# Kernel optimization log

Hardware: AMD Instinct MI355X
Metric: run time of the kernel (lower is better)

The kernel has to match this reference:

```python
import jax, jax.numpy as jnp
import numpy as np

NUM_QUBITS = 12
NUM_LAYERS = 4
N_CLASSES = 10
BATCH = 512
BN_EPS = 1e-5


def _apply_1q(state, U, wire):
    """Apply a 1-qubit gate U on `wire`. state: (B,)+(2,)*n; U: (2,2) or (B,2,2)."""
    state = jnp.moveaxis(state, wire + 1, -1)
    if U.ndim == 3:
        out = jnp.einsum('bij,b...j->b...i', U, state)
    else:
        out = jnp.einsum('ij,b...j->b...i', U, state)
    return jnp.moveaxis(out, -1, wire + 1)


def _apply_cnot(state, ctrl, tgt):
    s = jnp.moveaxis(state, (ctrl + 1, tgt + 1), (-2, -1))
    # where control bit == 1, flip the target axis
    s = jnp.concatenate([s[..., 0:1, :], s[..., 1:2, ::-1]], axis=-2)
    return jnp.moveaxis(s, (-2, -1), (ctrl + 1, tgt + 1))


def _rot(phi, theta, omega):
    """PennyLane Rot(phi, theta, omega) = RZ(omega) RY(theta) RZ(phi)."""
    c = jnp.cos(theta / 2)
    s = jnp.sin(theta / 2)
    row0 = jnp.stack([jnp.exp(-1j * (phi + omega) / 2) * c,
                      -jnp.exp(1j * (phi - omega) / 2) * s])
    row1 = jnp.stack([jnp.exp(-1j * (phi - omega) / 2) * s,
                      jnp.exp(1j * (phi + omega) / 2) * c])
    return jnp.stack([row0, row1]).astype(jnp.complex64)


def _circuit(x, weights):
    """Batched state-vector sim of the data-reuploading VQC.
    x: (B, n_qubits) angles; weights: (L, n_qubits, 3). Returns (B, N_CLASSES) <Z_i>."""
    B = x.shape[0]
    state = jnp.zeros((B,) + (2,) * NUM_QUBITS, jnp.complex64)
    state = state.at[(slice(None),) + (0,) * NUM_QUBITS].set(1.0)
    half = (x * 0.5).astype(jnp.float32)
    for l in range(NUM_LAYERS):
        w = weights[l]
        # angle embedding (RY(x_q) on each wire) -- batched gate, differs per sample
        for q in range(NUM_QUBITS):
            c = jnp.cos(half[:, q])
            s = jnp.sin(half[:, q])
            U = jnp.stack([jnp.stack([c, -s], -1),
                           jnp.stack([s, c], -1)], -2).astype(jnp.complex64)  # (B,2,2)
            state = _apply_1q(state, U, q)
        # one StronglyEntangling layer: Rot per wire (shared across batch)
        for q in range(NUM_QUBITS):
            state = _apply_1q(state, _rot(w[q, 0], w[q, 1], w[q, 2]), q)
        # ring of CNOTs (range 1)
        for q in range(NUM_QUBITS):
            state = _apply_cnot(state, q, (q + 1) % NUM_QUBITS)
    probs = jnp.abs(state) ** 2  # (B,)+(2,)*n, float32
    all_axes = tuple(range(1, NUM_QUBITS + 1))
    expz = []
    for i in range(N_CLASSES):
        axes = tuple(a for a in all_axes if a != i + 1)
        p = probs.sum(axis=axes)  # (B, 2) marginal of qubit i
        expz.append(p[:, 0] - p[:, 1])
    return jnp.stack(expz, axis=-1)  # (B, N_CLASSES)


def setup_inputs() -> dict:
    key = jax.random.key(0)
    k1, k2 = jax.random.split(key)
    x = jax.random.normal(k1, (BATCH, NUM_QUBITS), dtype=jnp.float32)
    weights = 0.01 * jax.random.uniform(k2, (NUM_LAYERS, NUM_QUBITS, 3), dtype=jnp.float32)
    bias = jnp.zeros((N_CLASSES,), jnp.float32)
    gamma = jnp.ones((N_CLASSES,), jnp.float32)
    beta = jnp.zeros((N_CLASSES,), jnp.float32)
    return {"x": x, "weights": weights, "bias": bias, "gamma": gamma, "beta": beta}


def reference(x, weights, bias, gamma, beta):
    expz = _circuit(x, weights)
    probs = jax.nn.softmax(expz + bias, axis=-1)
    # BatchNorm1d (training mode): biased batch statistics, affine
    mu = probs.mean(axis=0)
    var = probs.var(axis=0)
    return (probs - mu) / jnp.sqrt(var + BN_EPS) * gamma + beta
```

## Files before the change

kernel.cpp:

```cpp
#include <hip/hip_runtime.h>
#include <math.h>

#define NQ 12
#define NL 4
#define NC 10
#define NB 512
#define BN_EPS 1e-5f

typedef float v2f __attribute__((ext_vector_type(2)));

__device__ __forceinline__ void bfly(v2f& A, v2f& B,
    v2f c0, v2f c1, v2f c2, v2f c3, v2f c4, v2f c5, v2f c6, v2f c7)
{
    const v2f As = A.yx, Bs = B.yx;
    const v2f An = __builtin_elementwise_fma(c0, A,
                   __builtin_elementwise_fma(c1, As,
                   __builtin_elementwise_fma(c2, B, c3 * Bs)));
    const v2f Bn = __builtin_elementwise_fma(c4, A,
                   __builtin_elementwise_fma(c5, As,
                   __builtin_elementwise_fma(c6, B, c7 * Bs)));
    A = An; B = Bn;
}

__global__ __launch_bounds__(256) void vqc_kernel(
    const float* __restrict__ x, const float* __restrict__ w,
    const float* __restrict__ bias, float* __restrict__ probs)
{
    __shared__ v2f buf[2][4096];
    __shared__ __align__(16) float gm[48][16];
    __shared__ float red[4*NC];

    const int b = blockIdx.x;
    const int t = threadIdx.x;

    if (t < 48) {
        const int l = t / NQ, q = t % NQ;
        const float xq = 0.5f * x[b*NQ + q];
        const float cx = cosf(xq), sx = sinf(xq);
        const int wi = (l*NQ + q)*3;
        const float phi = w[wi], tht = w[wi+1], om = w[wi+2];
        const float ct = cosf(0.5f*tht), st = sinf(0.5f*tht);
        const float aa = 0.5f*(phi + om), dd = 0.5f*(phi - om);
        const float ca = cosf(aa), sa = sinf(aa);
        const float cd = cosf(dd), sd = sinf(dd);
        const float u00r =  ca*ct, u00i = -sa*ct;
        const float u01r = -cd*st, u01i = -sd*st;
        const float u10r =  cd*st, u10i = -sd*st;
        const float u11r =  ca*ct, u11i =  sa*ct;
        const float m00r = u00r*cx + u01r*sx, m00i = u00i*cx + u01i*sx;
        const float m01r = u01r*cx - u00r*sx, m01i = u01i*cx - u00i*sx;
        const float m10r = u10r*cx + u11r*sx, m10i = u10i*cx + u11i*sx;
        const float m11r = u11r*cx - u10r*sx, m11i = u11i*cx - u10i*sx;
        float* gp = gm[t];
        gp[0]  =  m00r; gp[1]  = m00r;
        gp[2]  = -m00i; gp[3]  = m00i;
        gp[4]  =  m01r; gp[5]  = m01r;
        gp[6]  = -m01i; gp[7]  = m01i;
        gp[8]  =  m10r; gp[9]  = m10r;
        gp[10] = -m10i; gp[11] = m10i;
        gp[12] =  m11r; gp[13] = m11r;
        gp[14] = -m11i; gp[15] = m11i;
    }
    __syncthreads();

    v2f a[16];
    #pragma unroll
    for (int r = 0; r < 16; ++r) a[r] = (v2f){0.f, 0.f};
    if (t == 0) a[0].x = 1.f;

    const int tl = t & 15, th4 = t >> 4;
    const int phit = t ^ th4;
    const int vAB = (th4 << 8) | (tl ^ (th4 * 17));
    const int wBC = (tl << 8) | ((th4 ^ tl) * 17);

    const unsigned b0_ = t & 1u, b1_ = (t>>1)&1u, b2_ = (t>>2)&1u, b3_ = (t>>3)&1u,
                   b4_ = (t>>4)&1u, b5_ = (t>>5)&1u, b6_ = (t>>6)&1u, b7_ = (t>>7)&1u;
    const unsigned P7 = b7_, P6 = P7^b6_, P5 = P6^b5_, P4 = P5^b4_,
                   P3 = P4^b3_, P2 = P3^b2_, P1 = P2^b1_, T = P1^b0_;
    const unsigned base_j = ((T ^ b7_) << 11) | (P6 << 10) | (P5 << 9) | (P4 << 8)
                          | (P3 << 7) | (P2 << 6) | (P1 << 5) | (T << 4)
                          | (T ? 0xFu : 0u);
    const unsigned rA = (base_j >> 8) & 15u;
    const unsigned tA = base_j & 255u;
    const unsigned baseCA = (rA << 8) | ((tA ^ (tA >> 4)) ^ (rA * 17u));

    #define STAGE(base) \
        _Pragma("unroll") \
        for (int g = 0; g < 4; ++g) { \
            const v2f* cp = (const v2f*)gm[(base) + 3 - g]; \
            const v2f c0=cp[0],c1=cp[1],c2=cp[2],c3=cp[3], \
                      c4=cp[4],c5=cp[5],c6=cp[6],c7=cp[7]; \
            const int bit = 1 << g; \
            _Pragma("unroll") \
            for (int r0 = 0; r0 < 16; ++r0) \
                if (!(r0 & bit)) bfly(a[r0], a[r0|bit], c0,c1,c2,c3,c4,c5,c6,c7); \
        }

    int pb = 0;
    #pragma unroll
    for (int l = 0; l < NL; ++l) {
        STAGE(l*12)
        {
            v2f* bp = buf[pb]; pb ^= 1;
            #pragma unroll
            for (int r = 0; r < 16; ++r) bp[vAB ^ (r*17)] = a[r];
            __syncthreads();
            #pragma unroll
            for (int r = 0; r < 16; ++r) a[r] = bp[(r<<8) | (phit ^ (r*17))];
        }

        STAGE(l*12 + 4)
        {
            v2f* bp = buf[pb]; pb ^= 1;
            #pragma unroll
            for (int r = 0; r < 16; ++r) bp[wBC ^ r] = a[r];
            __syncthreads();
            #pragma unroll
            for (int r = 0; r < 16; ++r) a[r] = bp[(r<<8) | (phit ^ (r*17))];
        }

        STAGE(l*12 + 8)
        if (l < NL-1) {
            v2f* bp = buf[pb]; pb ^= 1;
            #pragma unroll
            for (int r = 0; r < 16; ++r) {
                const unsigned k3 = (r>>3)&1u;
                const unsigned k2 = k3 ^ ((r>>2)&1u);
                const unsigned k1 = k2 ^ ((r>>1)&1u);
                const unsigned k0 = k1 ^ (r&1u);
                const unsigned K  = (k3<<3)|(k2<<2)|(k1<<1)|k0;
                const unsigned d  = K ^ (k0 * 0x888u);
                bp[baseCA ^ d] = a[r];
            }
            __syncthreads();
            #pragma unroll
            for (int r = 0; r < 16; ++r) a[r] = bp[(r<<8) | (phit ^ (r*17))];
        }
    }

    const float S0 = (T ^ b7_) ? -1.f : 1.f;
    const float S1 = P6 ? -1.f : 1.f;
    const float S2 = P5 ? -1.f : 1.f;
    const float S3 = P4 ? -1.f : 1.f;
    const float S4 = P3 ? -1.f : 1.f;
    const float S5 = P2 ? -1.f : 1.f;
    const float S6 = P1 ? -1.f : 1.f;
    const float S7 = T  ? -1.f : 1.f;
    const float S8 = T  ? -1.f : 1.f;
    const float S9 = T  ? -1.f : 1.f;

    float acc[NC];
    #pragma unroll
    for (int c = 0; c < NC; ++c) acc[c] = 0.f;
    #pragma unroll
    for (int r = 0; r < 16; ++r) {
        const float p = a[r].x*a[r].x + a[r].y*a[r].y;
        const int r3 = (r>>3)&1, r2 = (r>>2)&1, r1 = (r>>1)&1, r0b = r&1;
        const int par = r3 ^ r2 ^ r1 ^ r0b;
        acc[0] += (par        ? -S0 : S0) * p;
        acc[1] += S1 * p;
        acc[2] += S2 * p;
        acc[3] += S3 * p;
        acc[4] += S4 * p;
        acc[5] += S5 * p;
        acc[6] += S6 * p;
        acc[7] += S7 * p;
        acc[8] += (r3         ? -S8 : S8) * p;
        acc[9] += ((r3 ^ r2)  ? -S9 : S9) * p;
    }
    #pragma unroll
    for (int off = 32; off >= 1; off >>= 1) {
        #pragma unroll
        for (int c = 0; c < NC; ++c)
            acc[c] += __shfl_down(acc[c], off, 64);
    }
    const int wave = t >> 6, lane = t & 63;
    if (lane == 0) {
        #pragma unroll
        for (int c = 0; c < NC; ++c) red[wave*NC + c] = acc[c];
    }
    __syncthreads();
    if (t == 0) {
        float ez[NC];
        float mx = -1e30f;
        #pragma unroll
        for (int c = 0; c < NC; ++c) {
            ez[c] = red[c] + red[NC + c] + red[2*NC + c] + red[3*NC + c] + bias[c];
            mx = fmaxf(mx, ez[c]);
        }
        float sum = 0.f;
        #pragma unroll
        for (int c = 0; c < NC; ++c) { ez[c] = expf(ez[c] - mx); sum += ez[c]; }
        const float inv = 1.f / sum;
        #pragma unroll
        for (int c = 0; c < NC; ++c) probs[b*NC + c] = ez[c] * inv;
    }
}

__global__ __launch_bounds__(256) void bn_kernel(
    float* __restrict__ probs, const float* __restrict__ gamma,
    const float* __restrict__ beta)
{
    const int c = blockIdx.x;
    const int t = threadIdx.x;
    const float v0 = probs[t*NC + c];
    const float v1 = probs[(t + 256)*NC + c];
    float s  = v0 + v1;
    float ss = v0*v0 + v1*v1;
    #pragma unroll
    for (int off = 32; off >= 1; off >>= 1) {
        s  += __shfl_down(s,  off, 64);
        ss += __shfl_down(ss, off, 64);
    }
    __shared__ float sm[8];
    __shared__ float stat[2];
    const int wave = t >> 6, lane = t & 63;
    if (lane == 0) { sm[wave] = s; sm[4 + wave] = ss; }
    __syncthreads();
    if (t == 0) {
        const float S  = sm[0] + sm[1] + sm[2] + sm[3];
        const float SS = sm[4] + sm[5] + sm[6] + sm[7];
        const float mu  = S * (1.f/512.f);
        const float var = SS * (1.f/512.f) - mu*mu;
        stat[0] = mu;
        stat[1] = 1.f / sqrtf(var + BN_EPS);
    }
    __syncthreads();
    const float mu = stat[0], inv = stat[1];
    const float g = gamma[c], bt = beta[c];
    probs[t*NC + c]         = (v0 - mu) * inv * g + bt;
    probs[(t + 256)*NC + c] = (v1 - mu) * inv * g + bt;
}

extern "C" void kernel_launch(void* const* d_in, const int* in_sizes, int n_in,
                              void* d_out, int out_size, void* d_ws, size_t ws_size,
                              hipStream_t stream) {
    const float* x     = (const float*)d_in[0];
    const float* w     = (const float*)d_in[1];
    const float* bias  = (const float*)d_in[2];
    const float* gamma = (const float*)d_in[3];
    const float* beta  = (const float*)d_in[4];
    float* out = (float*)d_out;

    vqc_kernel<<<NB, 256, 0, stream>>>(x, w, bias, out);
    bn_kernel<<<NC, 256, 0, stream>>>(out, gamma, beta);
}
```

Baseline: 85.75 us.

## Use 512 threads per sample and precompute fused gates in a separate kernel

The state-vector simulation now runs with 512 threads per block, each holding 8 amplitudes instead of 16, so qubits are processed in groups of three with four LDS transposes per layer and new swizzle patterns. The per-sample fused gate matrices are computed by a new gates_kernel into workspace and read from global memory, rather than computed by 48 threads while the rest of the block waits. This aims to cut register pressure, raise occupancy and remove the serial gate-setup phase. In exchange it adds a kernel launch, a global round trip for gate coefficients and one more barrier-separated shuffle per layer.

```diff
diff --git a/kernel.cpp b/kernel.cpp
--- a/kernel.cpp
+++ b/kernel.cpp
@@ -22,142 +22,164 @@
     A = An; B = Bn;
 }
 
-__global__ __launch_bounds__(256) void vqc_kernel(
+__global__ __launch_bounds__(256) void gates_kernel(
     const float* __restrict__ x, const float* __restrict__ w,
-    const float* __restrict__ bias, float* __restrict__ probs)
+    float* __restrict__ gates)
+{
+    const int idx = blockIdx.x * 256 + threadIdx.x;
+    if (idx >= NB * 48) return;
+    const int b = idx / 48, g = idx % 48;
+    const int q = g % NQ;
+    const float xq = 0.5f * x[b*NQ + q];
+    const float cx = cosf(xq), sx = sinf(xq);
+    const int wi = g*3;
+    const float phi = w[wi], tht = w[wi+1], om = w[wi+2];
+    const float ct = cosf(0.5f*tht), st = sinf(0.5f*tht);
+    const float aa = 0.5f*(phi + om), dd = 0.5f*(phi - om);
+    const float ca = cosf(aa), sa = sinf(aa);
+    const float cd = cosf(dd), sd = sinf(dd);
+    const float u00r =  ca*ct, u00i = -sa*ct;
+    const float u01r = -cd*st, u01i = -sd*st;
+    const float u10r =  cd*st, u10i = -sd*st;
+    const float u11r =  ca*ct, u11i =  sa*ct;
+    const float m00r = u00r*cx + u01r*sx, m00i = u00i*cx + u01i*sx;
+    const float m01r = u01r*cx - u00r*sx, m01i = u01i*cx - u00i*sx;
+    const float m10r = u10r*cx + u11r*sx, m10i = u10i*cx + u11i*sx;
+    const float m11r = u11r*cx - u10r*sx, m11i = u11i*cx - u10i*sx;
+    float* gp = gates + (size_t)idx * 16;
+    gp[0]  =  m00r; gp[1]  = m00r;  gp[2]  = -m00i; gp[3]  = m00i;
+    gp[4]  =  m01r; gp[5]  = m01r;  gp[6]  = -m01i; gp[7]  = m01i;
+    gp[8]  =  m10r; gp[9]  = m10r;  gp[10] = -m10i; gp[11] = m10i;
+    gp[12] =  m11r; gp[13] = m11r;  gp[14] = -m11i; gp[15] = m11i;
+}
+
+__device__ __forceinline__ unsigned slotA(unsigned j) {
+    const unsigned v = j >> 9, x = (j & 511u) ^ (73u * v);
+    return (v << 9) | (x ^ (x >> 4));
+}
+__device__ __forceinline__ unsigned dA(int r) {
+    const unsigned p  = (0x96u >> r) & 1u;
+    const unsigned e2 = ((unsigned)r >> 2) & 1u;
+    const unsigned e1 = e2 ^ (((unsigned)r >> 1) & 1u);
+    const unsigned e0 = e1 ^ ((unsigned)r & 1u);
+    return (p << 11) | (e2 << 2) | (e1 << 1) | e0;
+}
+
+__global__ __launch_bounds__(512, 4) void vqc_kernel(
+    const float* __restrict__ gates, const float* __restrict__ bias,
+    float* __restrict__ probs)
 {
     __shared__ v2f buf[2][4096];
-    __shared__ __align__(16) float gm[48][16];
-    __shared__ float red[4*NC];
+    __shared__ float red[8*NC];
 
     const int b = blockIdx.x;
     const int t = threadIdx.x;
-
-    if (t < 48) {
-        const int l = t / NQ, q = t % NQ;
-        const float xq = 0.5f * x[b*NQ + q];
-        const float cx = cosf(xq), sx = sinf(xq);
-        const int wi = (l*NQ + q)*3;
-        const float phi = w[wi], tht = w[wi+1], om = w[wi+2];
-        const float ct = cosf(0.5f*tht), st = sinf(0.5f*tht);
-        const float aa = 0.5f*(phi + om), dd = 0.5f*(phi - om);
-        const float ca = cosf(aa), sa = sinf(aa);
-        const float cd = cosf(dd), sd = sinf(dd);
-        const float u00r =  ca*ct, u00i = -sa*ct;
-        const float u01r = -cd*st, u01i = -sd*st;
-        const float u10r =  cd*st, u10i = -sd*st;
-        const float u11r =  ca*ct, u11i =  sa*ct;
-        const float m00r = u00r*cx + u01r*sx, m00i = u00i*cx + u01i*sx;
-        const float m01r = u01r*cx - u00r*sx, m01i = u01i*cx - u00i*sx;
-        const float m10r = u10r*cx + u11r*sx, m10i = u10i*cx + u11i*sx;
-        const float m11r = u11r*cx - u10r*sx, m11i = u11i*cx - u10i*sx;
-        float* gp = gm[t];
-        gp[0]  =  m00r; gp[1]  = m00r;
-        gp[2]  = -m00i; gp[3]  = m00i;
-        gp[4]  =  m01r; gp[5]  = m01r;
-        gp[6]  = -m01i; gp[7]  = m01i;
-        gp[8]  =  m10r; gp[9]  = m10r;
-        gp[10] = -m10i; gp[11] = m10i;
-        gp[12] =  m11r; gp[13] = m11r;
-        gp[14] = -m11i; gp[15] = m11i;
-    }
-    __syncthreads();
-
-    v2f a[16];
-    #pragma unroll
-    for (int r = 0; r < 16; ++r) a[r] = (v2f){0.f, 0.f};
+    const v2f* gcp = (const v2f*)(gates + (size_t)b * 768);
+
+    const int w = t >> 6, lane = t & 63;
+    const int lane53 = (t >> 3) & 7, lane20 = t & 7;
+    const unsigned baseAB = ((unsigned)w << 9) | ((unsigned)lane ^ (73u * w));
+    const unsigned baseBC = ((unsigned)lane53 << 9)
+                          | ((((unsigned)w << 6) | (unsigned)lane20) ^ (73u * lane53));
+    const unsigned baseCD = ((unsigned)lane20 << 9)
+                          | ((((unsigned)w << 6) | ((unsigned)lane53 << 3)) ^ (73u * lane20));
+
+    const unsigned t8 = (t >> 8) & 1u;
+    const unsigned Q8 = t8;
+    const unsigned Q7 = Q8 ^ ((t >> 7) & 1u);
+    const unsigned Q6 = Q7 ^ ((t >> 6) & 1u);
+    const unsigned Q5 = Q6 ^ ((t >> 5) & 1u);
+    const unsigned Q4 = Q5 ^ ((t >> 4) & 1u);
+    const unsigned Q3 = Q4 ^ ((t >> 3) & 1u);
+    const unsigned Q2 = Q3 ^ ((t >> 2) & 1u);
+    const unsigned Q1 = Q2 ^ ((t >> 1) & 1u);
+    const unsigned Q0 = Q1 ^ (t & 1u);
+    const unsigned base_j = ((Q0 ^ t8) << 11) | (Q7 << 10) | (Q6 << 9) | (Q5 << 8)
+                          | (Q4 << 7) | (Q3 << 6) | (Q2 << 5) | (Q1 << 4) | (Q0 * 0xFu);
+    const unsigned baseDA = slotA(base_j);
+
+    v2f a[8];
+    #pragma unroll
+    for (int r = 0; r < 8; ++r) a[r] = (v2f){0.f, 0.f};
     if (t == 0) a[0].x = 1.f;
 
-    const int tl = t & 15, th4 = t >> 4;
-    const int phit = t ^ th4;
-    const int vAB = (th4 << 8) | (tl ^ (th4 * 17));
-    const int wBC = (tl << 8) | ((th4 ^ tl) * 17);
-
-    const unsigned b0_ = t & 1u, b1_ = (t>>1)&1u, b2_ = (t>>2)&1u, b3_ = (t>>3)&1u,
-                   b4_ = (t>>4)&1u, b5_ = (t>>5)&1u, b6_ = (t>>6)&1u, b7_ = (t>>7)&1u;
-    const unsigned P7 = b7_, P6 = P7^b6_, P5 = P6^b5_, P4 = P5^b4_,
-                   P3 = P4^b3_, P2 = P3^b2_, P1 = P2^b1_, T = P1^b0_;
-    const unsigned base_j = ((T ^ b7_) << 11) | (P6 << 10) | (P5 << 9) | (P4 << 8)
-                          | (P3 << 7) | (P2 << 6) | (P1 << 5) | (T << 4)
-                          | (T ? 0xFu : 0u);
-    const unsigned rA = (base_j >> 8) & 15u;
-    const unsigned tA = base_j & 255u;
-    const unsigned baseCA = (rA << 8) | ((tA ^ (tA >> 4)) ^ (rA * 17u));
-
-    #define STAGE(base) \
+    #define GATE(gi, bit) { \
+        const v2f* cp = gcp + (gi)*8; \
+        const v2f c0=cp[0],c1=cp[1],c2=cp[2],c3=cp[3], \
+                  c4=cp[4],c5=cp[5],c6=cp[6],c7=cp[7]; \
         _Pragma("unroll") \
-        for (int g = 0; g < 4; ++g) { \
-            const v2f* cp = (const v2f*)gm[(base) + 3 - g]; \
-            const v2f c0=cp[0],c1=cp[1],c2=cp[2],c3=cp[3], \
-                      c4=cp[4],c5=cp[5],c6=cp[6],c7=cp[7]; \
-            const int bit = 1 << g; \
-            _Pragma("unroll") \
-            for (int r0 = 0; r0 < 16; ++r0) \
-                if (!(r0 & bit)) bfly(a[r0], a[r0|bit], c0,c1,c2,c3,c4,c5,c6,c7); \
-        }
+        for (int r0 = 0; r0 < 8; ++r0) \
+            if (!(r0 & (bit))) bfly(a[r0], a[r0|(bit)], c0,c1,c2,c3,c4,c5,c6,c7); \
+    }
+    #define STAGE3(base) GATE((base)+2, 1) GATE((base)+1, 2) GATE((base)+0, 4)
 
     int pb = 0;
     #pragma unroll
     for (int l = 0; l < NL; ++l) {
-        STAGE(l*12)
+        STAGE3(l*12 + 0)
         {
             v2f* bp = buf[pb]; pb ^= 1;
             #pragma unroll
-            for (int r = 0; r < 16; ++r) bp[vAB ^ (r*17)] = a[r];
-            __syncthreads();
-            #pragma unroll
-            for (int r = 0; r < 16; ++r) a[r] = bp[(r<<8) | (phit ^ (r*17))];
-        }
-
-        STAGE(l*12 + 4)
+            for (int r = 0; r < 8; ++r) bp[baseAB ^ ((unsigned)r << 6)] = a[r];
+            __syncthreads();
+            #pragma unroll
+            for (int r = 0; r < 8; ++r)
+                a[r] = bp[((unsigned)r << 9) | ((unsigned)t ^ (73u * r))];
+        }
+        STAGE3(l*12 + 3)
         {
             v2f* bp = buf[pb]; pb ^= 1;
             #pragma unroll
-            for (int r = 0; r < 16; ++r) bp[wBC ^ r] = a[r];
-            __syncthreads();
-            #pragma unroll
-            for (int r = 0; r < 16; ++r) a[r] = bp[(r<<8) | (phit ^ (r*17))];
-        }
-
-        STAGE(l*12 + 8)
+            for (int r = 0; r < 8; ++r) bp[baseBC ^ ((unsigned)r << 3)] = a[r];
+            __syncthreads();
+            #pragma unroll
+            for (int r = 0; r < 8; ++r)
+                a[r] = bp[((unsigned)r << 9) | ((unsigned)t ^ (73u * r))];
+        }
+        STAGE3(l*12 + 6)
+        {
+            v2f* bp = buf[pb]; pb ^= 1;
+            #pragma unroll
+            for (int r = 0; r < 8; ++r) bp[baseCD ^ (unsigned)r] = a[r];
+            __syncthreads();
+            #pragma unroll
+            for (int r = 0; r < 8; ++r)
+                a[r] = bp[((unsigned)r << 9) | ((unsigned)t ^ (73u * r))];
+        }
+        STAGE3(l*12 + 9)
         if (l < NL-1) {
             v2f* bp = buf[pb]; pb ^= 1;
             #pragma unroll
-            for (int r = 0; r < 16; ++r) {
-                const unsigned k3 = (r>>3)&1u;
-                const unsigned k2 = k3 ^ ((r>>2)&1u);
-                const unsigned k1 = k2 ^ ((r>>1)&1u);
-                const unsigned k0 = k1 ^ (r&1u);
-                const unsigned K  = (k3<<3)|(k2<<2)|(k1<<1)|k0;
-                const unsigned d  = K ^ (k0 * 0x888u);
-                bp[baseCA ^ d] = a[r];
+            for (int r = 0; r < 8; ++r) bp[baseDA ^ slotA(dA(r))] = a[r];
+            __syncthreads();
+            #pragma unroll
+            for (int r = 0; r < 8; ++r) {
+                const unsigned xx = (unsigned)t ^ (73u * r);
+                a[r] = bp[((unsigned)r << 9) | (xx ^ (xx >> 4))];
             }
-            __syncthreads();
-            #pragma unroll
-            for (int r = 0; r < 16; ++r) a[r] = bp[(r<<8) | (phit ^ (r*17))];
-        }
-    }
-
-    const float S0 = (T ^ b7_) ? -1.f : 1.f;
-    const float S1 = P6 ? -1.f : 1.f;
-    const float S2 = P5 ? -1.f : 1.f;
-    const float S3 = P4 ? -1.f : 1.f;
-    const float S4 = P3 ? -1.f : 1.f;
-    const float S5 = P2 ? -1.f : 1.f;
-    const float S6 = P1 ? -1.f : 1.f;
-    const float S7 = T  ? -1.f : 1.f;
-    const float S8 = T  ? -1.f : 1.f;
-    const float S9 = T  ? -1.f : 1.f;
+        }
+    }
+
+    const float S0 = (Q0 ^ t8) ? -1.f : 1.f;
+    const float S1 = Q7 ? -1.f : 1.f;
+    const float S2 = Q6 ? -1.f : 1.f;
+    const float S3 = Q5 ? -1.f : 1.f;
+    const float S4 = Q4 ? -1.f : 1.f;
+    const float S5 = Q3 ? -1.f : 1.f;
+    const float S6 = Q2 ? -1.f : 1.f;
+    const float S7 = Q1 ? -1.f : 1.f;
+    const float S8 = Q0 ? -1.f : 1.f;
+    const float S9 = Q0 ? -1.f : 1.f;
 
     float acc[NC];
     #pragma unroll
     for (int c = 0; c < NC; ++c) acc[c] = 0.f;
     #pragma unroll
-    for (int r = 0; r < 16; ++r) {
+    for (int r = 0; r < 8; ++r) {
         const float p = a[r].x*a[r].x + a[r].y*a[r].y;
-        const int r3 = (r>>3)&1, r2 = (r>>2)&1, r1 = (r>>1)&1, r0b = r&1;
-        const int par = r3 ^ r2 ^ r1 ^ r0b;
-        acc[0] += (par        ? -S0 : S0) * p;
+        const int par = (0x96 >> r) & 1;
+        const int r2  = (r >> 2) & 1;
+        acc[0] += (par ? -S0 : S0) * p;
         acc[1] += S1 * p;
         acc[2] += S2 * p;
         acc[3] += S3 * p;
@@ -165,8 +187,8 @@
         acc[5] += S5 * p;
         acc[6] += S6 * p;
         acc[7] += S7 * p;
-        acc[8] += (r3         ? -S8 : S8) * p;
-        acc[9] += ((r3 ^ r2)  ? -S9 : S9) * p;
+        acc[8] += S8 * p;
+        acc[9] += (r2 ? -S9 : S9) * p;
     }
     #pragma unroll
     for (int off = 32; off >= 1; off >>= 1) {
@@ -174,10 +196,9 @@
         for (int c = 0; c < NC; ++c)
             acc[c] += __shfl_down(acc[c], off, 64);
     }
-    const int wave = t >> 6, lane = t & 63;
     if (lane == 0) {
         #pragma unroll
-        for (int c = 0; c < NC; ++c) red[wave*NC + c] = acc[c];
+        for (int c = 0; c < NC; ++c) red[w*NC + c] = acc[c];
     }
     __syncthreads();
     if (t == 0) {
@@ -185,7 +206,10 @@
         float mx = -1e30f;
         #pragma unroll
         for (int c = 0; c < NC; ++c) {
-            ez[c] = red[c] + red[NC + c] + red[2*NC + c] + red[3*NC + c] + bias[c];
+            float s = 0.f;
+            #pragma unroll
+            for (int k = 0; k < 8; ++k) s += red[k*NC + c];
+            ez[c] = s + bias[c];
             mx = fmaxf(mx, ez[c]);
         }
         float sum = 0.f;
@@ -214,8 +238,8 @@
     }
     __shared__ float sm[8];
     __shared__ float stat[2];
-    const int wave = t >> 6, lane = t & 63;
-    if (lane == 0) { sm[wave] = s; sm[4 + wave] = ss; }
+    const int wave = t >> 6, lanei = t & 63;
+    if (lanei == 0) { sm[wave] = s; sm[4 + wave] = ss; }
     __syncthreads();
     if (t == 0) {
         const float S  = sm[0] + sm[1] + sm[2] + sm[3];
@@ -240,8 +264,10 @@
     const float* bias  = (const float*)d_in[2];
     const float* gamma = (const float*)d_in[3];
     const float* beta  = (const float*)d_in[4];
-    float* out = (float*)d_out;
-
-    vqc_kernel<<<NB, 256, 0, stream>>>(x, w, bias, out);
+    float* out   = (float*)d_out;
+    float* gates = (float*)d_ws;
+
+    gates_kernel<<<(NB*48 + 255)/256, 256, 0, stream>>>(x, w, gates);
+    vqc_kernel<<<NB, 512, 0, stream>>>(gates, bias, out);
     bn_kernel<<<NC, 256, 0, stream>>>(out, gamma, beta);
 }
```

After: 91.80 us. +7.1%, slower.
